# Optimization experiments

Hardware: AMD Instinct MI355X
Metric: run time of the kernel (lower is better)

## Reference

```python
import jax, jax.numpy as jnp
import numpy as np

NUM_HEADS = 8
DIM_HEAD = 48
SCALE = DIM_HEAD ** -0.5


def setup_inputs() -> dict:
    key = jax.random.key(0)
    k1, k2, k3 = jax.random.split(key, 3)
    B, N, D = 4, 2048, 384
    inner = NUM_HEADS * DIM_HEAD  # 384
    x = jax.random.normal(k1, (B, N, D), dtype=jnp.float32)
    # store weights in [in, out] layout (equivalent to torch Linear W.T)
    Wqkv = jax.random.normal(k2, (D, 3 * inner), dtype=jnp.float32) * (D ** -0.5)
    Wproj = jax.random.normal(k3, (inner, D), dtype=jnp.float32) * (inner ** -0.5)
    bproj = jnp.zeros((D,), dtype=jnp.float32)
    return {"x": x, "Wqkv": Wqkv, "Wproj": Wproj, "bproj": bproj}


def reference(x, Wqkv, Wproj, bproj):
    B, N, D = x.shape
    h, dh = NUM_HEADS, DIM_HEAD
    C = h * dh
    # fused QKV projection (qkv_bias=False)
    qkv = (x @ Wqkv).reshape(B, N, 3, h, dh)
    q = qkv[:, :, 0].transpose(0, 2, 1, 3)  # [B, h, N, dh]
    k = qkv[:, :, 1].transpose(0, 2, 1, 3)
    v = qkv[:, :, 2].transpose(0, 2, 1, 3)
    # naive attention: materialize [B, h, N, N] scores
    sim = jnp.einsum("bhqd,bhkd->bhqk", q, k) * SCALE
    attn = jax.nn.softmax(sim, axis=-1)
    out = jnp.einsum("bhqk,bhkd->bhqd", attn, v)  # [B, h, N, dh]
    out = out.transpose(0, 2, 1, 3).reshape(B, N, C)
    return out @ Wproj + bproj
```

## Files before the change

kernel.cpp:

```cpp
#include <hip/hip_runtime.h>
#include <hip/hip_bf16.h>


typedef _Float16 f16x8 __attribute__((ext_vector_type(8)));
typedef _Float16 f16x4 __attribute__((ext_vector_type(4)));
typedef float    f32x4 __attribute__((ext_vector_type(4)));
typedef float    f32x16 __attribute__((ext_vector_type(16)));

#define QSCL 0.20822035963448658f

__global__ __launch_bounds__(256) void prep(const float4* __restrict__ x,
                                            const float* __restrict__ wq,
                                            const float* __restrict__ wp,
                                            f16x4* __restrict__ xh4,
                                            _Float16* __restrict__ wqt,
                                            _Float16* __restrict__ wpt)
{
    const int i = blockIdx.x * 256 + threadIdx.x;
    const int T = 1536 * 256;
    #pragma unroll
    for (int rep = 0; rep < 2; rep++) {
        const int j = i + rep * T;
        const float4 t = x[j];
        f16x4 h;
        h[0] = (_Float16)t.x; h[1] = (_Float16)t.y;
        h[2] = (_Float16)t.z; h[3] = (_Float16)t.w;
        xh4[j] = h;
    }
    for (int j = i; j < 384 * 1152; j += T) {
        const int n = j / 384, k = j - n * 384;
        wqt[j] = (_Float16)wq[(size_t)k * 1152 + n];
    }
    for (int j = i; j < 384 * 384; j += T) {
        const int n = j / 384, k = j - n * 384;
        wpt[j] = (_Float16)wp[(size_t)k * 384 + n];
    }
}

__global__ __launch_bounds__(256) void qkv_f16(const _Float16* __restrict__ A,
                                               const _Float16* __restrict__ Bt,
                                               _Float16* __restrict__ qh,
                                               _Float16* __restrict__ kh,
                                               _Float16* __restrict__ vt)
{
    __shared__ _Float16 As[128][72];
    __shared__ _Float16 Bs[64][72];
    const int tid = threadIdx.x;
    const int w = tid >> 6, lane = tid & 63, cl = lane & 15, quad = lane >> 4;
    const int bm = blockIdx.x, bn = blockIdx.y;

    f32x4 acc[2][4];
    const f32x4 z4 = {0.f, 0.f, 0.f, 0.f};
    #pragma unroll
    for (int mi = 0; mi < 2; mi++)
        #pragma unroll
        for (int t = 0; t < 4; t++) acc[mi][t] = z4;

    const int ar = tid >> 3, ac = (tid & 7) * 8;
    const _Float16* Ag = A  + (size_t)(bm * 128 + ar) * 384 + ac;
    const _Float16* Bg = Bt + (size_t)(bn * 64  + ar) * 384 + ac;

    for (int k0 = 0; k0 < 384; k0 += 64) {
        __syncthreads();
        #pragma unroll
        for (int j = 0; j < 4; j++) {
            *(f16x8*)&As[ar + 32 * j][ac] = *(const f16x8*)(Ag + (size_t)(32 * j) * 384 + k0);
        }
        #pragma unroll
        for (int j = 0; j < 2; j++) {
            *(f16x8*)&Bs[ar + 32 * j][ac] = *(const f16x8*)(Bg + (size_t)(32 * j) * 384 + k0);
        }
        __syncthreads();
        #pragma unroll
        for (int kh2 = 0; kh2 < 2; kh2++) {
            f16x8 bf[4];
            #pragma unroll
            for (int t = 0; t < 4; t++)
                bf[t] = *(const f16x8*)&Bs[t * 16 + cl][kh2 * 32 + quad * 8];
            #pragma unroll
            for (int mi = 0; mi < 2; mi++) {
                const f16x8 af = *(const f16x8*)&As[w * 32 + mi * 16 + cl][kh2 * 32 + quad * 8];
                #pragma unroll
                for (int t = 0; t < 4; t++)
                    acc[mi][t] = __builtin_amdgcn_mfma_f32_16x16x32_f16(af, bf[t], acc[mi][t], 0, 0, 0);
            }
        }
    }

    const int s = (bn * 64) / 384;
    #pragma unroll
    for (int t = 0; t < 4; t++) {
        const int col  = bn * 64 + t * 16 + cl - s * 384;
        const int head = col / 48, d = col - head * 48;
        #pragma unroll
        for (int mi = 0; mi < 2; mi++) {
            #pragma unroll
            for (int r = 0; r < 4; r++) {
                const int row = bm * 128 + w * 32 + mi * 16 + quad * 4 + r;
                const int b = row >> 11, n = row & 2047;
                const int bh = b * 8 + head;
                const float v = acc[mi][t][r];
                if (s == 0)
                    qh[(size_t)(bh * 2048 + n) * 48 + d] = (_Float16)(v * QSCL);
                else if (s == 1)
                    kh[(size_t)(bh * 2048 + n) * 48 + d] = (_Float16)v;
                else
                    vt[(size_t)(bh * 48 + d) * 2048 + n] = (_Float16)v;
            }
        }
    }
}

__global__ __launch_bounds__(256) void attn_f16(const _Float16* __restrict__ qh,
                                                const _Float16* __restrict__ kh,
                                                const _Float16* __restrict__ vt,
                                                _Float16* __restrict__ ab)
{
    __shared__ _Float16 Ks[64][56];
    __shared__ _Float16 Vts[64][72];
    __shared__ _Float16 Ps[128][72];
    const int tid = threadIdx.x;
    const int w = tid >> 6, lane = tid & 63, ln = lane & 31, h = lane >> 5;
    const int bh = blockIdx.x, qt = blockIdx.y;

    for (int i = tid; i < 16 * 72; i += 256) {
        const int r = 48 + i / 72, c = i - (i / 72) * 72;
        Vts[r][c] = (r == 48) ? (_Float16)1.0f : (_Float16)0.0f;
    }

    f16x8 qf[3];
    {
        const _Float16* qp = qh + (size_t)(bh * 2048 + qt * 128 + w * 32 + ln) * 48 + 8 * h;
        qf[0] = *(const f16x8*)qp;
        qf[1] = *(const f16x8*)(qp + 16);
        qf[2] = *(const f16x8*)(qp + 32);
    }

    f32x16 o0 = {0.f}, o1 = {0.f};
    #pragma unroll
    for (int r = 0; r < 16; r++) { o0[r] = 0.f; o1[r] = 0.f; }

    const _Float16* kbase = kh + (size_t)bh * 2048 * 48;
    const _Float16* vbase = vt + (size_t)bh * 48 * 2048;

    const int kr0 = tid / 6,         kc0 = (tid % 6) * 8;
    const int kid1 = tid + 256;
    const int kr1 = kid1 / 6,        kc1 = (kid1 % 6) * 8;
    const int vr0 = tid >> 3,        vc0 = (tid & 7) * 8;
    const int vr1 = (tid + 256) >> 3;
    const _Float16* ks0 = kbase + (size_t)kr0 * 48 + kc0;
    const _Float16* ks1 = kbase + (size_t)kr1 * 48 + kc1;
    const _Float16* vs0 = vbase + (size_t)vr0 * 2048 + vc0;
    const _Float16* vs1 = vbase + (size_t)vr1 * 2048 + vc0;

    for (int kt = 0; kt < 2048; kt += 64) {
        __syncthreads();
        *(f16x8*)&Ks[kr0][kc0]  = *(const f16x8*)(ks0 + (size_t)kt * 48);
        *(f16x8*)&Vts[vr0][vc0] = *(const f16x8*)(vs0 + kt);
        if (tid < 128) {
            *(f16x8*)&Ks[kr1][kc1]  = *(const f16x8*)(ks1 + (size_t)kt * 48);
            *(f16x8*)&Vts[vr1][vc0] = *(const f16x8*)(vs1 + kt);
        }
        __syncthreads();

        f32x16 s0 = o0, s1 = o0;
        #pragma unroll
        for (int r = 0; r < 16; r++) { s0[r] = 0.f; s1[r] = 0.f; }
        #pragma unroll
        for (int i = 0; i < 3; i++) {
            const f16x8 ka0 = *(const f16x8*)&Ks[ln][16 * i + 8 * h];
            s0 = __builtin_amdgcn_mfma_f32_32x32x16_f16(ka0, qf[i], s0, 0, 0, 0);
            const f16x8 ka1 = *(const f16x8*)&Ks[32 + ln][16 * i + 8 * h];
            s1 = __builtin_amdgcn_mfma_f32_32x32x16_f16(ka1, qf[i], s1, 0, 0, 0);
        }

        #pragma unroll
        for (int q = 0; q < 4; q++) {
            f16x4 pk;
            pk[0] = (_Float16)exp2f(s0[4 * q + 0]);
            pk[1] = (_Float16)exp2f(s0[4 * q + 1]);
            pk[2] = (_Float16)exp2f(s0[4 * q + 2]);
            pk[3] = (_Float16)exp2f(s0[4 * q + 3]);
            *(f16x4*)&Ps[w * 32 + ln][8 * q + 4 * h] = pk;
            f16x4 pk1;
            pk1[0] = (_Float16)exp2f(s1[4 * q + 0]);
            pk1[1] = (_Float16)exp2f(s1[4 * q + 1]);
            pk1[2] = (_Float16)exp2f(s1[4 * q + 2]);
            pk1[3] = (_Float16)exp2f(s1[4 * q + 3]);
            *(f16x4*)&Ps[w * 32 + ln][32 + 8 * q + 4 * h] = pk1;
        }

        #pragma unroll
        for (int i = 0; i < 4; i++) {
            const f16x8 pa = *(const f16x8*)&Ps[w * 32 + ln][16 * i + 8 * h];
            const f16x8 v0 = *(const f16x8*)&Vts[ln][16 * i + 8 * h];
            o0 = __builtin_amdgcn_mfma_f32_32x32x16_f16(pa, v0, o0, 0, 0, 0);
            const f16x8 v1 = *(const f16x8*)&Vts[32 + ln][16 * i + 8 * h];
            o1 = __builtin_amdgcn_mfma_f32_32x32x16_f16(pa, v1, o1, 0, 0, 0);
        }
    }

    const int b = bh >> 3, hd = bh & 7;
    #pragma unroll
    for (int r = 0; r < 16; r++) {
        const float lr = __shfl(o1[r], (lane & 32) + 16);
        const float inv = 1.f / lr;
        const int q = qt * 128 + w * 32 + (r & 3) + 8 * (r >> 2) + 4 * h;
        _Float16* orow = ab + (size_t)(b * 2048 + q) * 384 + hd * 48;
        orow[ln] = (_Float16)(o0[r] * inv);
        if (ln < 16) orow[32 + ln] = (_Float16)(o1[r] * inv);
    }
}

__global__ __launch_bounds__(256) void proj_f16(const _Float16* __restrict__ A,
                                                const _Float16* __restrict__ Bt,
                                                const float* __restrict__ bias,
                                                float* __restrict__ out)
{
    __shared__ _Float16 As[64][72];
    __shared__ _Float16 Bs[64][72];
    const int tid = threadIdx.x;
    const int w = tid >> 6, lane = tid & 63, cl = lane & 15, quad = lane >> 4;
    const int bm = blockIdx.x, bn = blockIdx.y;

    f32x4 acc[4];
    const f32x4 z4 = {0.f, 0.f, 0.f, 0.f};
    #pragma unroll
    for (int t = 0; t < 4; t++) acc[t] = z4;

    const int ar = tid >> 3, ac = (tid & 7) * 8;
    const _Float16* Ag = A  + (size_t)(bm * 64 + ar) * 384 + ac;
    const _Float16* Bg = Bt + (size_t)(bn * 64 + ar) * 384 + ac;

    for (int k0 = 0; k0 < 384; k0 += 64) {
        __syncthreads();
        #pragma unroll
        for (int j = 0; j < 2; j++) {
            *(f16x8*)&As[ar + 32 * j][ac] = *(const f16x8*)(Ag + (size_t)(32 * j) * 384 + k0);
            *(f16x8*)&Bs[ar + 32 * j][ac] = *(const f16x8*)(Bg + (size_t)(32 * j) * 384 + k0);
        }
        __syncthreads();
        #pragma unroll
        for (int kh2 = 0; kh2 < 2; kh2++) {
            const f16x8 af = *(const f16x8*)&As[w * 16 + cl][kh2 * 32 + quad * 8];
            #pragma unroll
            for (int t = 0; t < 4; t++) {
                const f16x8 bf = *(const f16x8*)&Bs[t * 16 + cl][kh2 * 32 + quad * 8];
                acc[t] = __builtin_amdgcn_mfma_f32_16x16x32_f16(af, bf, acc[t], 0, 0, 0);
            }
        }
    }

    #pragma unroll
    for (int t = 0; t < 4; t++) {
        const int col = bn * 64 + t * 16 + cl;
        const float bv = bias[col];
        #pragma unroll
        for (int r = 0; r < 4; r++) {
            const int row = bm * 64 + w * 16 + quad * 4 + r;
            out[(size_t)row * 384 + col] = acc[t][r] + bv;
        }
    }
}

extern "C" void kernel_launch(void* const* d_in, const int* in_sizes, int n_in,
                              void* d_out, int out_size, void* d_ws, size_t ws_size,
                              hipStream_t stream) {
    const float* x     = (const float*)d_in[0];
    const float* Wqkv  = (const float*)d_in[1];
    const float* Wproj = (const float*)d_in[2];
    const float* bproj = (const float*)d_in[3];
    float* out = (float*)d_out;

    char* ws = (char*)d_ws;
    _Float16* xh     = (_Float16*)(ws + 0);
    _Float16* wqkvt  = (_Float16*)(ws + 6291456);
    _Float16* wprojt = (_Float16*)(ws + 7176192);
    _Float16* qh     = (_Float16*)(ws + 7471104);
    _Float16* kh     = (_Float16*)(ws + 13762560);
    _Float16* vt     = (_Float16*)(ws + 20054016);
    _Float16* ab     = (_Float16*)(ws + 26345472);

    prep<<<1536, 256, 0, stream>>>((const float4*)x, Wqkv, Wproj,
                                   (f16x4*)xh, wqkvt, wprojt);
    qkv_f16<<<dim3(64, 18), 256, 0, stream>>>(xh, wqkvt, qh, kh, vt);
    attn_f16<<<dim3(32, 16), 256, 0, stream>>>(qh, kh, vt, ab);
    proj_f16<<<dim3(128, 6), 256, 0, stream>>>(ab, wprojt, bproj, out);
}
```

Before: 160.6 us.

## Register-prefetch next tiles in GEMM and attention loops; tiled weight transpose

Adds register double-buffering to the qkv, attention and projection kernels: the next K/V or A/B tile is loaded from global memory right after the barrier, so the load overlaps with the MFMA work on the current tile. Rewrites the prep kernel to transpose the weight matrices through a shared-memory tile, making both reads and writes coalesced instead of strided. The x conversion is given to a dedicated set of blocks in a smaller grid. The prefetch costs extra VGPRs, which may lower occupancy.

```diff
diff --git a/kernel.cpp b/kernel.cpp
--- a/kernel.cpp
+++ b/kernel.cpp
@@ -16,24 +16,42 @@
                                             _Float16* __restrict__ wqt,
                                             _Float16* __restrict__ wpt)
 {
-    const int i = blockIdx.x * 256 + threadIdx.x;
-    const int T = 1536 * 256;
-    #pragma unroll
-    for (int rep = 0; rep < 2; rep++) {
-        const int j = i + rep * T;
-        const float4 t = x[j];
-        f16x4 h;
-        h[0] = (_Float16)t.x; h[1] = (_Float16)t.y;
-        h[2] = (_Float16)t.z; h[3] = (_Float16)t.w;
-        xh4[j] = h;
-    }
-    for (int j = i; j < 384 * 1152; j += T) {
-        const int n = j / 384, k = j - n * 384;
-        wqt[j] = (_Float16)wq[(size_t)k * 1152 + n];
-    }
-    for (int j = i; j < 384 * 384; j += T) {
-        const int n = j / 384, k = j - n * 384;
-        wpt[j] = (_Float16)wp[(size_t)k * 384 + n];
+    __shared__ _Float16 t[64][65];
+    const int blk = blockIdx.x, tid = threadIdx.x;
+    if (blk < 144) {
+        const float* src; _Float16* dst; int Nn, k0, n0;
+        if (blk < 108) {
+            src = wq; dst = wqt; Nn = 1152;
+            k0 = (blk % 6) * 64; n0 = (blk / 6) * 64;
+        } else {
+            const int b2 = blk - 108;
+            src = wp; dst = wpt; Nn = 384;
+            k0 = (b2 % 6) * 64; n0 = (b2 / 6) * 64;
+        }
+        #pragma unroll
+        for (int i = 0; i < 16; i++) {
+            const int id = tid + i * 256;
+            const int k = id >> 6, n = id & 63;
+            t[k][n] = (_Float16)src[(size_t)(k0 + k) * Nn + n0 + n];
+        }
+        __syncthreads();
+        #pragma unroll
+        for (int i = 0; i < 16; i++) {
+            const int id = tid + i * 256;
+            const int n = id >> 6, k = id & 63;
+            dst[(size_t)(n0 + n) * 384 + k0 + k] = t[k][n];
+        }
+    } else {
+        const int base = (blk - 144) * 3072;
+        #pragma unroll
+        for (int r = 0; r < 12; r++) {
+            const int j = base + r * 256 + tid;
+            const float4 tt = x[j];
+            f16x4 h;
+            h[0] = (_Float16)tt.x; h[1] = (_Float16)tt.y;
+            h[2] = (_Float16)tt.z; h[3] = (_Float16)tt.w;
+            xh4[j] = h;
+        }
     }
 }
 
@@ -60,17 +78,27 @@
     const _Float16* Ag = A  + (size_t)(bm * 128 + ar) * 384 + ac;
     const _Float16* Bg = Bt + (size_t)(bn * 64  + ar) * 384 + ac;
 
+    f16x8 pa[4], pb[2];
+    #pragma unroll
+    for (int j = 0; j < 4; j++) pa[j] = *(const f16x8*)(Ag + (size_t)(32 * j) * 384);
+    #pragma unroll
+    for (int j = 0; j < 2; j++) pb[j] = *(const f16x8*)(Bg + (size_t)(32 * j) * 384);
+
     for (int k0 = 0; k0 < 384; k0 += 64) {
         __syncthreads();
         #pragma unroll
-        for (int j = 0; j < 4; j++) {
-            *(f16x8*)&As[ar + 32 * j][ac] = *(const f16x8*)(Ag + (size_t)(32 * j) * 384 + k0);
-        }
-        #pragma unroll
-        for (int j = 0; j < 2; j++) {
-            *(f16x8*)&Bs[ar + 32 * j][ac] = *(const f16x8*)(Bg + (size_t)(32 * j) * 384 + k0);
-        }
-        __syncthreads();
+        for (int j = 0; j < 4; j++) *(f16x8*)&As[ar + 32 * j][ac] = pa[j];
+        #pragma unroll
+        for (int j = 0; j < 2; j++) *(f16x8*)&Bs[ar + 32 * j][ac] = pb[j];
+        __syncthreads();
+        if (k0 + 64 < 384) {
+            #pragma unroll
+            for (int j = 0; j < 4; j++)
+                pa[j] = *(const f16x8*)(Ag + (size_t)(32 * j) * 384 + k0 + 64);
+            #pragma unroll
+            for (int j = 0; j < 2; j++)
+                pb[j] = *(const f16x8*)(Bg + (size_t)(32 * j) * 384 + k0 + 64);
+        }
         #pragma unroll
         for (int kh2 = 0; kh2 < 2; kh2++) {
             f16x8 bf[4];
@@ -136,7 +164,7 @@
         qf[2] = *(const f16x8*)(qp + 32);
     }
 
-    f32x16 o0 = {0.f}, o1 = {0.f};
+    f32x16 o0, o1;
     #pragma unroll
     for (int r = 0; r < 16; r++) { o0[r] = 0.f; o1[r] = 0.f; }
 
@@ -153,17 +181,30 @@
     const _Float16* vs0 = vbase + (size_t)vr0 * 2048 + vc0;
     const _Float16* vs1 = vbase + (size_t)vr1 * 2048 + vc0;
 
+    f16x8 rk0 = *(const f16x8*)ks0;
+    f16x8 rv0 = *(const f16x8*)vs0;
+    f16x8 rk1, rv1;
+    if (tid < 128) { rk1 = *(const f16x8*)ks1; rv1 = *(const f16x8*)vs1; }
+
     for (int kt = 0; kt < 2048; kt += 64) {
         __syncthreads();
-        *(f16x8*)&Ks[kr0][kc0]  = *(const f16x8*)(ks0 + (size_t)kt * 48);
-        *(f16x8*)&Vts[vr0][vc0] = *(const f16x8*)(vs0 + kt);
+        *(f16x8*)&Ks[kr0][kc0]  = rk0;
+        *(f16x8*)&Vts[vr0][vc0] = rv0;
         if (tid < 128) {
-            *(f16x8*)&Ks[kr1][kc1]  = *(const f16x8*)(ks1 + (size_t)kt * 48);
-            *(f16x8*)&Vts[vr1][vc0] = *(const f16x8*)(vs1 + kt);
-        }
-        __syncthreads();
-
-        f32x16 s0 = o0, s1 = o0;
+            *(f16x8*)&Ks[kr1][kc1]  = rk1;
+            *(f16x8*)&Vts[vr1][vc0] = rv1;
+        }
+        __syncthreads();
+        if (kt + 64 < 2048) {
+            rk0 = *(const f16x8*)(ks0 + (size_t)(kt + 64) * 48);
+            rv0 = *(const f16x8*)(vs0 + kt + 64);
+            if (tid < 128) {
+                rk1 = *(const f16x8*)(ks1 + (size_t)(kt + 64) * 48);
+                rv1 = *(const f16x8*)(vs1 + kt + 64);
+            }
+        }
+
+        f32x16 s0, s1;
         #pragma unroll
         for (int r = 0; r < 16; r++) { s0[r] = 0.f; s1[r] = 0.f; }
         #pragma unroll
@@ -232,14 +273,28 @@
     const _Float16* Ag = A  + (size_t)(bm * 64 + ar) * 384 + ac;
     const _Float16* Bg = Bt + (size_t)(bn * 64 + ar) * 384 + ac;
 
+    f16x8 pa[2], pb[2];
+    #pragma unroll
+    for (int j = 0; j < 2; j++) {
+        pa[j] = *(const f16x8*)(Ag + (size_t)(32 * j) * 384);
+        pb[j] = *(const f16x8*)(Bg + (size_t)(32 * j) * 384);
+    }
+
     for (int k0 = 0; k0 < 384; k0 += 64) {
         __syncthreads();
         #pragma unroll
         for (int j = 0; j < 2; j++) {
-            *(f16x8*)&As[ar + 32 * j][ac] = *(const f16x8*)(Ag + (size_t)(32 * j) * 384 + k0);
-            *(f16x8*)&Bs[ar + 32 * j][ac] = *(const f16x8*)(Bg + (size_t)(32 * j) * 384 + k0);
-        }
-        __syncthreads();
+            *(f16x8*)&As[ar + 32 * j][ac] = pa[j];
+            *(f16x8*)&Bs[ar + 32 * j][ac] = pb[j];
+        }
+        __syncthreads();
+        if (k0 + 64 < 384) {
+            #pragma unroll
+            for (int j = 0; j < 2; j++) {
+                pa[j] = *(const f16x8*)(Ag + (size_t)(32 * j) * 384 + k0 + 64);
+                pb[j] = *(const f16x8*)(Bg + (size_t)(32 * j) * 384 + k0 + 64);
+            }
+        }
         #pragma unroll
         for (int kh2 = 0; kh2 < 2; kh2++) {
             const f16x8 af = *(const f16x8*)&As[w * 16 + cl][kh2 * 32 + quad * 8];
@@ -281,8 +336,8 @@
     _Float16* vt     = (_Float16*)(ws + 20054016);
     _Float16* ab     = (_Float16*)(ws + 26345472);
 
-    prep<<<1536, 256, 0, stream>>>((const float4*)x, Wqkv, Wproj,
-                                   (f16x4*)xh, wqkvt, wprojt);
+    prep<<<400, 256, 0, stream>>>((const float4*)x, Wqkv, Wproj,
+                                  (f16x4*)xh, wqkvt, wprojt);
     qkv_f16<<<dim3(64, 18), 256, 0, stream>>>(xh, wqkvt, qh, kh, vt);
     attn_f16<<<dim3(32, 16), 256, 0, stream>>>(qh, kh, vt, ab);
     proj_f16<<<dim3(128, 6), 256, 0, stream>>>(ab, wprojt, bproj, out);
```

Result: faster. 154.7 us (-3.7%).
